# Optimization experiments

Hardware: AMD Instinct MI355X
Metric: run time of the kernel (lower is better)

The kernel has to match this reference:

```python
import jax, jax.numpy as jnp
import numpy as np

N, E, D, H = 50000, 800000, 128, 4

def setup_inputs() -> dict:
    key = jax.random.key(0)
    ks = jax.random.split(key, 6)
    x = jax.random.normal(ks[0], (N, D), dtype=jnp.float32)
    edge_index = jax.random.randint(ks[1], (2, E), 0, N, dtype=jnp.int64)
    W = jax.random.normal(ks[2], (D, H * D), dtype=jnp.float32) * (1.0 / np.sqrt(D))
    att_src = jax.random.normal(ks[3], (H, D), dtype=jnp.float32) * 0.1
    att_dst = jax.random.normal(ks[4], (H, D), dtype=jnp.float32) * 0.1
    bias = jnp.zeros((D,), dtype=jnp.float32)
    gamma = jnp.ones((D,), dtype=jnp.float32)
    beta = jnp.zeros((D,), dtype=jnp.float32)
    return {"x": x, "edge_index": edge_index, "W": W, "att_src": att_src,
            "att_dst": att_dst, "bias": bias, "gamma": gamma, "beta": beta}

def reference(x, edge_index, W, att_src, att_dst, bias, gamma, beta):
    src, dst = edge_index[0], edge_index[1]
    # GATConv: linear transform per head -> [N, H, D]
    xw = (x @ W).reshape(N, H, D)
    a_src = jnp.einsum('nhd,hd->nh', xw, att_src)  # [N, H]
    a_dst = jnp.einsum('nhd,hd->nh', xw, att_dst)  # [N, H]
    alpha = a_src[src] + a_dst[dst]                # [E, H]
    alpha = jax.nn.leaky_relu(alpha, negative_slope=0.2)
    # segment softmax over incoming edges of each dst node
    m = jax.ops.segment_max(alpha, dst, num_segments=N)   # [N, H]
    ex = jnp.exp(alpha - m[dst])                            # [E, H]
    denom = jax.ops.segment_sum(ex, dst, num_segments=N)   # [N, H]
    attn = ex / denom[dst]                                  # [E, H]
    msg = xw[src] * attn[:, :, None]                        # [E, H, D]
    agg = jax.ops.segment_sum(msg, dst, num_segments=N)    # [N, H, D]
    out = agg.mean(axis=1) + bias                           # concat=False: mean heads
    # LayerNorm (eps=1e-5)
    mu = out.mean(axis=-1, keepdims=True)
    var = out.var(axis=-1, keepdims=True)
    out = (out - mu) * jax.lax.rsqrt(var + 1e-5) * gamma + beta
    out = jax.nn.gelu(out, approximate=False)
    return out + x  # project is Identity (in_channels == out_channels)
```

## Files before the change

### kernel.cpp

```cpp
#include <hip/hip_runtime.h>
#include <hip/hip_bf16.h>
#include <hip/hip_fp16.h>
#include <math.h>

#define ND 128
#define NH 4
#define HD 512

typedef __attribute__((ext_vector_type(8))) short bf16x8;
typedef __attribute__((ext_vector_type(4))) float f32x4;

__device__ __forceinline__ unsigned pack_bf16(float a, float b) {
    unsigned ua = __float_as_uint(a), ub = __float_as_uint(b);
    ua = (ua + 0x7fffu + ((ua >> 16) & 1u)) >> 16;
    ub = (ub + 0x7fffu + ((ub >> 16) & 1u)) >> 16;
    return ua | (ub << 16);
}
__device__ __forceinline__ unsigned short bf16r(float a) {
    unsigned ua = __float_as_uint(a);
    return (unsigned short)((ua + 0x7fffu + ((ua >> 16) & 1u)) >> 16);
}
__device__ __forceinline__ float bflo(unsigned u) { return __uint_as_float(u << 16); }
__device__ __forceinline__ float bfhi(unsigned u) { return __uint_as_float(u & 0xffff0000u); }
__device__ __forceinline__ unsigned pack_half2(float a, float b) {
    __half ha = __float2half(a), hb = __float2half(b);
    return (unsigned)__half_as_ushort(ha) | ((unsigned)__half_as_ushort(hb) << 16);
}
__device__ __forceinline__ float2 h22f(unsigned u) {
    __half2 h = *(__half2*)&u;
    return __half22float2(h);
}

__global__ __launch_bounds__(256) void prep_misc(const float* __restrict__ W,
                                                 const float* __restrict__ att_src,
                                                 const float* __restrict__ att_dst,
                                                 unsigned short* __restrict__ Ws,
                                                 float* __restrict__ pt,
                                                 const int* __restrict__ dst,
                                                 int* __restrict__ cnt, int ne) {
    int b = blockIdx.x;
    if (b < 256) {
        int idx = b * 256 + threadIdx.x;
        int j = idx >> 9, K = idx & 511;
        int h = K >> 7, k = K & 127;
        Ws[idx] = bf16r(W[(size_t)k * HD + h * ND + j]);
    } else if (b == 256) {
        int k = threadIdx.x;
        if (k < ND) {
            for (int h = 0; h < NH; ++h) {
                float ps = 0.f, pd = 0.f;
                for (int d = 0; d < ND; ++d) {
                    float wv = W[(size_t)k * HD + h * ND + d];
                    ps = fmaf(wv, att_src[h * ND + d], ps);
                    pd = fmaf(wv, att_dst[h * ND + d], pd);
                }
                pt[h * ND + k] = ps;
                pt[(4 + h) * ND + k] = pd;
            }
        }
    } else {
        int e = (b - 257) * 256 + threadIdx.x;
        if (e < ne) atomicAdd(&cnt[dst[e]], 1);
    }
}

__global__ __launch_bounds__(256) void ka_scanA(const float* __restrict__ x,
                                                const float* __restrict__ pt,
                                                unsigned* __restrict__ xb,
                                                float* __restrict__ a_src,
                                                float* __restrict__ a_dst,
                                                const int* __restrict__ cnt,
                                                int* __restrict__ partial,
                                                int* __restrict__ bsum,
                                                int n, int nbA) {
    __shared__ float pl[8 * ND];
    __shared__ int sh[256];
    if ((int)blockIdx.x < nbA) {
        { int t = threadIdx.x; ((float4*)pl)[t] = ((const float4*)pt)[t]; }
        __syncthreads();
        int wave = (blockIdx.x * 256 + threadIdx.x) >> 6;
        int lane = threadIdx.x & 63;
        if (wave >= n) return;
        float2 xv = ((const float2*)(x + (size_t)wave * ND))[lane];
        xb[(size_t)wave * 64 + lane] = pack_bf16(xv.x, xv.y);
#pragma unroll
        for (int o = 0; o < 8; ++o) {
            float2 pv = ((const float2*)(pl + o * ND))[lane];
            float v = xv.x * pv.x + xv.y * pv.y;
#pragma unroll
            for (int off = 1; off < 64; off <<= 1) v += __shfl_xor(v, off);
            if (lane == 0) {
                if (o < 4) a_src[(size_t)wave * NH + o] = v;
                else       a_dst[(size_t)wave * NH + (o - 4)] = v;
            }
        }
    } else {
        int bid = blockIdx.x - nbA;
        int gid = bid * 256 + threadIdx.x;
        int v = (gid < n) ? cnt[gid] : 0;
        int val = v;
        sh[threadIdx.x] = val;
        __syncthreads();
#pragma unroll
        for (int off = 1; off < 256; off <<= 1) {
            int add = (threadIdx.x >= off) ? sh[threadIdx.x - off] : 0;
            __syncthreads();
            val += add;
            sh[threadIdx.x] = val;
            __syncthreads();
        }
        if (gid < n) partial[gid] = val - v;
        if (threadIdx.x == 255) bsum[bid] = val;
    }
}

__global__ __launch_bounds__(256) void scanBC(const int* __restrict__ partial,
                                              const int* __restrict__ bsum,
                                              int* __restrict__ starts,
                                              int* __restrict__ cursor,
                                              int n, int ne, int nb) {
    __shared__ int sh[256];
    int t = threadIdx.x;
    int v = (t < nb) ? bsum[t] : 0;
    int val = v;
    sh[t] = val;
    __syncthreads();
#pragma unroll
    for (int off = 1; off < 256; off <<= 1) {
        int add = (t >= off) ? sh[t - off] : 0;
        __syncthreads();
        val += add;
        sh[t] = val;
        __syncthreads();
    }
    int myoff = (blockIdx.x == 0) ? 0 : sh[blockIdx.x - 1];
    int gid = blockIdx.x * 256 + t;
    if (gid < n) {
        int s = partial[gid] + myoff;
        starts[gid] = s;
        cursor[gid] = s;
    }
    if (gid == 0) starts[n] = ne;
}

__global__ __launch_bounds__(256) void scatter_edges_w(const int* __restrict__ src,
                                                       const int* __restrict__ dst,
                                                       const float* __restrict__ a_src,
                                                       const float* __restrict__ a_dst,
                                                       int* __restrict__ cursor,
                                                       uint4* __restrict__ eperm, int ne) {
    int e = blockIdx.x * 256 + threadIdx.x;
    if (e < ne) {
        int s = src[e], t = dst[e];
        float4 as = *(const float4*)(a_src + (size_t)s * NH);
        float4 ad = *(const float4*)(a_dst + (size_t)t * NH);
        float A0 = as.x + ad.x, A1 = as.y + ad.y, A2 = as.z + ad.z, A3 = as.w + ad.w;
        A0 = (A0 > 0.f) ? A0 : 0.2f * A0;
        A1 = (A1 > 0.f) ? A1 : 0.2f * A1;
        A2 = (A2 > 0.f) ? A2 : 0.2f * A2;
        A3 = (A3 > 0.f) ? A3 : 0.2f * A3;
        float e0 = expf(A0), e1 = expf(A1), e2 = expf(A2), e3 = expf(A3);
        int pos = atomicAdd(&cursor[t], 1);
        uint4 ev;
        ev.x = (unsigned)s;
        ev.y = pack_half2(e0, e1);
        ev.z = pack_half2(e2, e3);
        ev.w = 0u;
        eperm[pos] = ev;
    }
}

#define FMA16()                                                            \
    { float f0 = bflo(xv.x), f1 = bfhi(xv.x), f2 = bflo(xv.y), f3 = bfhi(xv.y); \
      acc[0] = fmaf(w01.x, f0, acc[0]);  acc[1] = fmaf(w01.x, f1, acc[1]);  \
      acc[2] = fmaf(w01.x, f2, acc[2]);  acc[3] = fmaf(w01.x, f3, acc[3]);  \
      acc[4] = fmaf(w01.y, f0, acc[4]);  acc[5] = fmaf(w01.y, f1, acc[5]);  \
      acc[6] = fmaf(w01.y, f2, acc[6]);  acc[7] = fmaf(w01.y, f3, acc[7]);  \
      acc[8] = fmaf(w23.x, f0, acc[8]);  acc[9] = fmaf(w23.x, f1, acc[9]);  \
      acc[10] = fmaf(w23.x, f2, acc[10]); acc[11] = fmaf(w23.x, f3, acc[11]); \
      acc[12] = fmaf(w23.y, f0, acc[12]); acc[13] = fmaf(w23.y, f1, acc[13]); \
      acc[14] = fmaf(w23.y, f2, acc[14]); acc[15] = fmaf(w23.y, f3, acc[15]); }

__global__ __launch_bounds__(256) void node_agg_fused(
        const uint4* __restrict__ eperm, const int* __restrict__ starts,
        const uint2* __restrict__ xb2, const unsigned short* __restrict__ Ws,
        const float* __restrict__ x, const float* __restrict__ bias,
        const float* __restrict__ gamma, const float* __restrict__ beta,
        float* __restrict__ out, int n) {
    __shared__ char lds[16384];

    const int w = threadIdx.x >> 6;
    const int lane = threadIdx.x & 63;
    const int slot = lane & 31;
    const int half = lane >> 5;
    const int node0 = blockIdx.x * 16;

    for (int i = 0; i < 4; ++i) {
        const int nl = w * 4 + i;
        const int node = node0 + nl;
        int s0 = 0, s1 = 0;
        if (node < n) { s0 = starts[node]; s1 = starts[node + 1]; }

        float den0 = 0.f, den1 = 0.f, den2 = 0.f, den3 = 0.f;
        float acc[16];
#pragma unroll
        for (int j = 0; j < 16; ++j) acc[j] = 0.f;

        for (int base = s0; base < s1; base += 16) {
            int rem = s1 - base; if (rem > 16) rem = 16;
            uint4 ev = {0u, 0u, 0u, 0u};
            if (lane < rem) ev = eperm[base + lane];
            {
                float2 dl = h22f(ev.y), dh = h22f(ev.z);
                den0 += dl.x; den1 += dl.y; den2 += dh.x; den3 += dh.y;
            }
            if (rem == 16) {
#pragma unroll
                for (int pp = 0; pp < 8; ++pp) {
                    int j2 = 2 * pp + half;
                    int s = __shfl((int)ev.x, j2);
                    unsigned uy = __shfl(ev.y, j2);
                    unsigned uz = __shfl(ev.z, j2);
                    uint2 xv = xb2[(size_t)s * 32 + slot];
                    float2 w01 = h22f(uy), w23 = h22f(uz);
                    FMA16();
                }
            } else {
                for (int jj = 0; jj < rem; jj += 2) {
                    int j2 = jj + half;
                    bool valid = (j2 < rem);
                    int j2c = valid ? j2 : jj;
                    int s = __shfl((int)ev.x, j2c);
                    unsigned uy = __shfl(ev.y, j2c);
                    unsigned uz = __shfl(ev.z, j2c);
                    uint2 xv = xb2[(size_t)s * 32 + slot];
                    float2 w01 = h22f(uy), w23 = h22f(uz);
                    float m = valid ? 1.f : 0.f;
                    w01.x *= m; w01.y *= m; w23.x *= m; w23.y *= m;
                    FMA16();
                }
            }
        }

#pragma unroll
        for (int off = 1; off < 64; off <<= 1) {
            den0 += __shfl_xor(den0, off);
            den1 += __shfl_xor(den1, off);
            den2 += __shfl_xor(den2, off);
            den3 += __shfl_xor(den3, off);
        }
        float i0 = (den0 > 0.f) ? 0.25f / den0 : 0.f;
        float i1 = (den1 > 0.f) ? 0.25f / den1 : 0.f;
        float i2 = (den2 > 0.f) ? 0.25f / den2 : 0.f;
        float i3 = (den3 > 0.f) ? 0.25f / den3 : 0.f;

        float v[16];
#pragma unroll
        for (int f = 0; f < 4; ++f) {
            v[0 + f]  = acc[0 + f]  * i0;
            v[4 + f]  = acc[4 + f]  * i1;
            v[8 + f]  = acc[8 + f]  * i2;
            v[12 + f] = acc[12 + f] * i3;
        }
#pragma unroll
        for (int j = 0; j < 16; ++j) v[j] += __shfl_xor(v[j], 32);

#pragma unroll
        for (int hh = 0; hh < 2; ++hh) {
            int h = half * 2 + hh;
            int Kb = (h * ND + slot * 4) * 2;
            int boff = nl * 1024 + ((Kb & ~15) ^ ((nl & 7) << 4)) + (Kb & 8);
            uint2 val;
            val.x = pack_bf16(v[h * 4 + 0], v[h * 4 + 1]);
            val.y = pack_bf16(v[h * 4 + 2], v[h * 4 + 3]);
            *(uint2*)(lds + boff) = val;
        }
    }
    __syncthreads();

    const int g16 = lane >> 4;
    const int e16 = lane & 15;
    f32x4 cacc[2];
    cacc[0] = (f32x4){0.f, 0.f, 0.f, 0.f};
    cacc[1] = (f32x4){0.f, 0.f, 0.f, 0.f};
#pragma unroll
    for (int t = 0; t < 16; ++t) {
        int K0 = t * 32 + 8 * g16;
        bf16x8 a = *(const bf16x8*)(lds + e16 * 1024 + ((K0 * 2) ^ ((e16 & 7) << 4)));
#pragma unroll
        for (int c2 = 0; c2 < 2; ++c2) {
            int c = w * 2 + c2;
            bf16x8 b = *(const bf16x8*)(Ws + (size_t)(c * 16 + e16) * HD + K0);
            cacc[c2] = __builtin_amdgcn_mfma_f32_16x16x32_bf16(a, b, cacc[c2], 0, 0, 0);
        }
    }
    __syncthreads();

    float* C = (float*)lds;
#pragma unroll
    for (int c2 = 0; c2 < 2; ++c2)
#pragma unroll
        for (int ri = 0; ri < 4; ++ri)
            C[(g16 * 4 + ri) * 128 + (w * 2 + c2) * 16 + e16] = cacc[c2][ri];
    __syncthreads();

    float2 bv = ((const float2*)bias)[lane];
    float2 gv = ((const float2*)gamma)[lane];
    float2 tb = ((const float2*)beta)[lane];
    for (int i = 0; i < 4; ++i) {
        int row = w * 4 + i;
        int grow = node0 + row;
        if (grow >= n) break;
        float2 c2v = ((float2*)(C + row * 128))[lane];
        c2v.x += bv.x; c2v.y += bv.y;
        float s = c2v.x + c2v.y, s2 = c2v.x * c2v.x + c2v.y * c2v.y;
#pragma unroll
        for (int off = 1; off < 64; off <<= 1) {
            s += __shfl_xor(s, off);
            s2 += __shfl_xor(s2, off);
        }
        float mu = s * (1.0f / ND);
        float var = s2 * (1.0f / ND) - mu * mu;
        var = fmaxf(var, 0.0f);
        float inv = rsqrtf(var + 1e-5f);
        float2 xres = ((const float2*)(x + (size_t)grow * ND))[lane];
        float y0 = (c2v.x - mu) * inv * gv.x + tb.x;
        float y1 = (c2v.y - mu) * inv * gv.y + tb.y;
        y0 = 0.5f * y0 * (1.0f + erff(y0 * 0.70710678118654752f)) + xres.x;
        y1 = 0.5f * y1 * (1.0f + erff(y1 * 0.70710678118654752f)) + xres.y;
        float2 ov = {y0, y1};
        ((float2*)(out + (size_t)grow * ND))[lane] = ov;
    }
}

extern "C" void kernel_launch(void* const* d_in, const int* in_sizes, int n_in,
                              void* d_out, int out_size, void* d_ws, size_t ws_size,
                              hipStream_t stream) {
    const float* x       = (const float*)d_in[0];
    const int*   edge    = (const int*)d_in[1];
    const float* W       = (const float*)d_in[2];
    const float* att_src = (const float*)d_in[3];
    const float* att_dst = (const float*)d_in[4];
    const float* bias    = (const float*)d_in[5];
    const float* gamma   = (const float*)d_in[6];
    const float* beta    = (const float*)d_in[7];
    float* out = (float*)d_out;

    const int n  = in_sizes[0] / ND;
    const int ne = in_sizes[1] / 2;
    const int* src = edge;
    const int* dst = edge + ne;

    const int nb  = (n + 255) / 256;
    const int nbA = (n + 3) / 4;

    char* wsp = (char*)d_ws;
    unsigned* xb        = (unsigned*)wsp;        wsp += (size_t)n * 64 * sizeof(unsigned);
    unsigned short* Ws  = (unsigned short*)wsp;  wsp += (size_t)ND * HD * sizeof(short);
    float* pt      = (float*)wsp;               wsp += (size_t)8 * ND * sizeof(float);
    float* a_src   = (float*)wsp;               wsp += (size_t)n * NH * sizeof(float);
    float* a_dst   = (float*)wsp;               wsp += (size_t)n * NH * sizeof(float);
    uint4* eperm   = (uint4*)wsp;               wsp += (size_t)ne * sizeof(uint4);
    int*   cnt     = (int*)wsp;                 wsp += (size_t)n * sizeof(int);
    int*   partial = (int*)wsp;                 wsp += (size_t)n * sizeof(int);
    int*   bsum    = (int*)wsp;                 wsp += 256 * sizeof(int);
    int*   starts  = (int*)wsp;                 wsp += (size_t)(n + 1) * sizeof(int);
    int*   cursor  = (int*)wsp;                 wsp += (size_t)n * sizeof(int);

    (void)hipMemsetAsync(cnt, 0, (size_t)n * sizeof(int), stream);

    prep_misc<<<257 + (ne + 255) / 256, 256, 0, stream>>>(W, att_src, att_dst,
                                                          Ws, pt, dst, cnt, ne);

    ka_scanA<<<nbA + nb, 256, 0, stream>>>(x, pt, xb, a_src, a_dst,
                                           cnt, partial, bsum, n, nbA);

    scanBC<<<nb, 256, 0, stream>>>(partial, bsum, starts, cursor, n, ne, nb);

    scatter_edges_w<<<(ne + 255) / 256, 256, 0, stream>>>(src, dst, a_src, a_dst,
                                                          cursor, eperm, ne);

    node_agg_fused<<<(n + 15) / 16, 256, 0, stream>>>(eperm, starts, (const uint2*)xb,
                                                      Ws, x, bias, gamma, beta, out, n);
}
```

Measured before the change: 256.2 us.

## Split fused aggregation+GEMM into separate node aggregation and MFMA GEMM kernels

The fused kernel that aggregated 16 nodes per block into LDS and then ran an MFMA projection is split in two. node_agg now handles one node per wave and writes the bf16 aggregated features to a global buffer. A separate gemm_out kernel then does a 64-row MFMA GEMM with LayerNorm, GELU and the residual in registers. This removes the per-block syncs and LDS staging, and each wave finishes independently instead of waiting on degree imbalance within a block. The cost is an extra n×512 bf16 round trip through global memory (about 51 MB) plus one more launch. The exp in the edge scatter is also switched to the fast __expf.

```diff
diff --git a/kernel.cpp b/kernel.cpp
--- a/kernel.cpp
+++ b/kernel.cpp
@@ -159,7 +159,7 @@
         A1 = (A1 > 0.f) ? A1 : 0.2f * A1;
         A2 = (A2 > 0.f) ? A2 : 0.2f * A2;
         A3 = (A3 > 0.f) ? A3 : 0.2f * A3;
-        float e0 = expf(A0), e1 = expf(A1), e2 = expf(A2), e3 = expf(A3);
+        float e0 = __expf(A0), e1 = __expf(A1), e2 = __expf(A2), e3 = __expf(A3);
         int pos = atomicAdd(&cursor[t], 1);
         uint4 ev;
         ev.x = (unsigned)s;
@@ -181,155 +181,156 @@
       acc[12] = fmaf(w23.y, f0, acc[12]); acc[13] = fmaf(w23.y, f1, acc[13]); \
       acc[14] = fmaf(w23.y, f2, acc[14]); acc[15] = fmaf(w23.y, f3, acc[15]); }
 
-__global__ __launch_bounds__(256) void node_agg_fused(
-        const uint4* __restrict__ eperm, const int* __restrict__ starts,
-        const uint2* __restrict__ xb2, const unsigned short* __restrict__ Ws,
+__global__ __launch_bounds__(256) void node_agg(const uint4* __restrict__ eperm,
+                                                const int* __restrict__ starts,
+                                                const uint2* __restrict__ xb2,
+                                                unsigned* __restrict__ u, int n) {
+    int node = (blockIdx.x * 256 + threadIdx.x) >> 6;
+    int lane = threadIdx.x & 63;
+    if (node >= n) return;
+    const int slot = lane & 31;
+    const int half = lane >> 5;
+
+    int s0 = starts[node], s1 = starts[node + 1];
+
+    float den0 = 0.f, den1 = 0.f, den2 = 0.f, den3 = 0.f;
+    float acc[16];
+#pragma unroll
+    for (int j = 0; j < 16; ++j) acc[j] = 0.f;
+
+    for (int base = s0; base < s1; base += 16) {
+        int rem = s1 - base; if (rem > 16) rem = 16;
+        uint4 ev = {0u, 0u, 0u, 0u};
+        if (lane < rem) ev = eperm[base + lane];
+        {
+            float2 dl = h22f(ev.y), dh = h22f(ev.z);
+            den0 += dl.x; den1 += dl.y; den2 += dh.x; den3 += dh.y;
+        }
+        if (rem == 16) {
+#pragma unroll
+            for (int pp = 0; pp < 8; ++pp) {
+                int j2 = 2 * pp + half;
+                int s = __shfl((int)ev.x, j2);
+                unsigned uy = __shfl(ev.y, j2);
+                unsigned uz = __shfl(ev.z, j2);
+                uint2 xv = xb2[(size_t)s * 32 + slot];
+                float2 w01 = h22f(uy), w23 = h22f(uz);
+                FMA16();
+            }
+        } else {
+            for (int jj = 0; jj < rem; jj += 2) {
+                int j2 = jj + half;
+                bool valid = (j2 < rem);
+                int j2c = valid ? j2 : jj;
+                int s = __shfl((int)ev.x, j2c);
+                unsigned uy = __shfl(ev.y, j2c);
+                unsigned uz = __shfl(ev.z, j2c);
+                uint2 xv = xb2[(size_t)s * 32 + slot];
+                float2 w01 = h22f(uy), w23 = h22f(uz);
+                float m = valid ? 1.f : 0.f;
+                w01.x *= m; w01.y *= m; w23.x *= m; w23.y *= m;
+                FMA16();
+            }
+        }
+    }
+
+#pragma unroll
+    for (int off = 1; off < 64; off <<= 1) {
+        den0 += __shfl_xor(den0, off);
+        den1 += __shfl_xor(den1, off);
+        den2 += __shfl_xor(den2, off);
+        den3 += __shfl_xor(den3, off);
+    }
+    float i0 = (den0 > 0.f) ? 0.25f / den0 : 0.f;
+    float i1 = (den1 > 0.f) ? 0.25f / den1 : 0.f;
+    float i2 = (den2 > 0.f) ? 0.25f / den2 : 0.f;
+    float i3 = (den3 > 0.f) ? 0.25f / den3 : 0.f;
+
+    float v[16];
+#pragma unroll
+    for (int f = 0; f < 4; ++f) {
+        v[0 + f]  = acc[0 + f]  * i0;
+        v[4 + f]  = acc[4 + f]  * i1;
+        v[8 + f]  = acc[8 + f]  * i2;
+        v[12 + f] = acc[12 + f] * i3;
+    }
+#pragma unroll
+    for (int j = 0; j < 16; ++j) v[j] += __shfl_xor(v[j], 32);
+
+#pragma unroll
+    for (int hh = 0; hh < 2; ++hh) {
+        int h = half * 2 + hh;
+        uint2 val;
+        val.x = pack_bf16(v[h * 4 + 0], v[h * 4 + 1]);
+        val.y = pack_bf16(v[h * 4 + 2], v[h * 4 + 3]);
+        ((uint2*)u)[(size_t)node * 128 + h * 32 + slot] = val;
+    }
+}
+
+__global__ __launch_bounds__(256) void gemm_out(
+        const unsigned short* __restrict__ u, const unsigned short* __restrict__ Ws,
         const float* __restrict__ x, const float* __restrict__ bias,
         const float* __restrict__ gamma, const float* __restrict__ beta,
         float* __restrict__ out, int n) {
-    __shared__ char lds[16384];
-
-    const int w = threadIdx.x >> 6;
-    const int lane = threadIdx.x & 63;
-    const int slot = lane & 31;
-    const int half = lane >> 5;
-    const int node0 = blockIdx.x * 16;
-
-    for (int i = 0; i < 4; ++i) {
-        const int nl = w * 4 + i;
-        const int node = node0 + nl;
-        int s0 = 0, s1 = 0;
-        if (node < n) { s0 = starts[node]; s1 = starts[node + 1]; }
-
-        float den0 = 0.f, den1 = 0.f, den2 = 0.f, den3 = 0.f;
-        float acc[16];
-#pragma unroll
-        for (int j = 0; j < 16; ++j) acc[j] = 0.f;
-
-        for (int base = s0; base < s1; base += 16) {
-            int rem = s1 - base; if (rem > 16) rem = 16;
-            uint4 ev = {0u, 0u, 0u, 0u};
-            if (lane < rem) ev = eperm[base + lane];
-            {
-                float2 dl = h22f(ev.y), dh = h22f(ev.z);
-                den0 += dl.x; den1 += dl.y; den2 += dh.x; den3 += dh.y;
-            }
-            if (rem == 16) {
-#pragma unroll
-                for (int pp = 0; pp < 8; ++pp) {
-                    int j2 = 2 * pp + half;
-                    int s = __shfl((int)ev.x, j2);
-                    unsigned uy = __shfl(ev.y, j2);
-                    unsigned uz = __shfl(ev.z, j2);
-                    uint2 xv = xb2[(size_t)s * 32 + slot];
-                    float2 w01 = h22f(uy), w23 = h22f(uz);
-                    FMA16();
-                }
-            } else {
-                for (int jj = 0; jj < rem; jj += 2) {
-                    int j2 = jj + half;
-                    bool valid = (j2 < rem);
-                    int j2c = valid ? j2 : jj;
-                    int s = __shfl((int)ev.x, j2c);
-                    unsigned uy = __shfl(ev.y, j2c);
-                    unsigned uz = __shfl(ev.z, j2c);
-                    uint2 xv = xb2[(size_t)s * 32 + slot];
-                    float2 w01 = h22f(uy), w23 = h22f(uz);
-                    float m = valid ? 1.f : 0.f;
-                    w01.x *= m; w01.y *= m; w23.x *= m; w23.y *= m;
-                    FMA16();
-                }
-            }
-        }
-
-#pragma unroll
-        for (int off = 1; off < 64; off <<= 1) {
-            den0 += __shfl_xor(den0, off);
-            den1 += __shfl_xor(den1, off);
-            den2 += __shfl_xor(den2, off);
-            den3 += __shfl_xor(den3, off);
-        }
-        float i0 = (den0 > 0.f) ? 0.25f / den0 : 0.f;
-        float i1 = (den1 > 0.f) ? 0.25f / den1 : 0.f;
-        float i2 = (den2 > 0.f) ? 0.25f / den2 : 0.f;
-        float i3 = (den3 > 0.f) ? 0.25f / den3 : 0.f;
-
-        float v[16];
-#pragma unroll
-        for (int f = 0; f < 4; ++f) {
-            v[0 + f]  = acc[0 + f]  * i0;
-            v[4 + f]  = acc[4 + f]  * i1;
-            v[8 + f]  = acc[8 + f]  * i2;
-            v[12 + f] = acc[12 + f] * i3;
-        }
-#pragma unroll
-        for (int j = 0; j < 16; ++j) v[j] += __shfl_xor(v[j], 32);
-
-#pragma unroll
-        for (int hh = 0; hh < 2; ++hh) {
-            int h = half * 2 + hh;
-            int Kb = (h * ND + slot * 4) * 2;
-            int boff = nl * 1024 + ((Kb & ~15) ^ ((nl & 7) << 4)) + (Kb & 8);
-            uint2 val;
-            val.x = pack_bf16(v[h * 4 + 0], v[h * 4 + 1]);
-            val.y = pack_bf16(v[h * 4 + 2], v[h * 4 + 3]);
-            *(uint2*)(lds + boff) = val;
-        }
-    }
-    __syncthreads();
-
-    const int g16 = lane >> 4;
-    const int e16 = lane & 15;
-    f32x4 cacc[2];
-    cacc[0] = (f32x4){0.f, 0.f, 0.f, 0.f};
-    cacc[1] = (f32x4){0.f, 0.f, 0.f, 0.f};
-#pragma unroll
-    for (int t = 0; t < 16; ++t) {
-        int K0 = t * 32 + 8 * g16;
-        bf16x8 a = *(const bf16x8*)(lds + e16 * 1024 + ((K0 * 2) ^ ((e16 & 7) << 4)));
-#pragma unroll
-        for (int c2 = 0; c2 < 2; ++c2) {
-            int c = w * 2 + c2;
-            bf16x8 b = *(const bf16x8*)(Ws + (size_t)(c * 16 + e16) * HD + K0);
-            cacc[c2] = __builtin_amdgcn_mfma_f32_16x16x32_bf16(a, b, cacc[c2], 0, 0, 0);
-        }
-    }
-    __syncthreads();
-
-    float* C = (float*)lds;
-#pragma unroll
-    for (int c2 = 0; c2 < 2; ++c2)
-#pragma unroll
-        for (int ri = 0; ri < 4; ++ri)
-            C[(g16 * 4 + ri) * 128 + (w * 2 + c2) * 16 + e16] = cacc[c2][ri];
-    __syncthreads();
-
-    float2 bv = ((const float2*)bias)[lane];
-    float2 gv = ((const float2*)gamma)[lane];
-    float2 tb = ((const float2*)beta)[lane];
-    for (int i = 0; i < 4; ++i) {
-        int row = w * 4 + i;
-        int grow = node0 + row;
-        if (grow >= n) break;
-        float2 c2v = ((float2*)(C + row * 128))[lane];
-        c2v.x += bv.x; c2v.y += bv.y;
-        float s = c2v.x + c2v.y, s2 = c2v.x * c2v.x + c2v.y * c2v.y;
-#pragma unroll
-        for (int off = 1; off < 64; off <<= 1) {
+    const int t = threadIdx.x;
+    const int w = t >> 6, l = t & 63;
+    const int e16 = l & 15, g16 = l >> 4;
+    const int row0 = blockIdx.x * 64 + w * 16;
+
+    int arow = row0 + e16; if (arow >= n) arow = n - 1;
+    const unsigned short* ap = u + (size_t)arow * HD + g16 * 8;
+    const unsigned short* bp[8];
+#pragma unroll
+    for (int c = 0; c < 8; ++c) bp[c] = Ws + (size_t)(c * 16 + e16) * HD + g16 * 8;
+
+    f32x4 acc[8];
+#pragma unroll
+    for (int c = 0; c < 8; ++c) acc[c] = (f32x4){0.f, 0.f, 0.f, 0.f};
+
+#pragma unroll 4
+    for (int ks = 0; ks < 16; ++ks) {
+        bf16x8 a = *(const bf16x8*)(ap + ks * 32);
+#pragma unroll
+        for (int c = 0; c < 8; ++c) {
+            bf16x8 b = *(const bf16x8*)(bp[c] + ks * 32);
+            acc[c] = __builtin_amdgcn_mfma_f32_16x16x32_bf16(a, b, acc[c], 0, 0, 0);
+        }
+    }
+
+    float bias_l[8], gam_l[8], bet_l[8];
+#pragma unroll
+    for (int c = 0; c < 8; ++c) {
+        bias_l[c] = bias[c * 16 + e16];
+        gam_l[c]  = gamma[c * 16 + e16];
+        bet_l[c]  = beta[c * 16 + e16];
+    }
+#pragma unroll
+    for (int ri = 0; ri < 4; ++ri) {
+        int grow = row0 + g16 * 4 + ri;
+        float val[8];
+        float s = 0.f, s2 = 0.f;
+#pragma unroll
+        for (int c = 0; c < 8; ++c) {
+            val[c] = acc[c][ri] + bias_l[c];
+            s += val[c]; s2 += val[c] * val[c];
+        }
+#pragma unroll
+        for (int off = 1; off < 16; off <<= 1) {
             s += __shfl_xor(s, off);
             s2 += __shfl_xor(s2, off);
         }
         float mu = s * (1.0f / ND);
-        float var = s2 * (1.0f / ND) - mu * mu;
-        var = fmaxf(var, 0.0f);
+        float var = fmaxf(s2 * (1.0f / ND) - mu * mu, 0.0f);
         float inv = rsqrtf(var + 1e-5f);
-        float2 xres = ((const float2*)(x + (size_t)grow * ND))[lane];
-        float y0 = (c2v.x - mu) * inv * gv.x + tb.x;
-        float y1 = (c2v.y - mu) * inv * gv.y + tb.y;
-        y0 = 0.5f * y0 * (1.0f + erff(y0 * 0.70710678118654752f)) + xres.x;
-        y1 = 0.5f * y1 * (1.0f + erff(y1 * 0.70710678118654752f)) + xres.y;
-        float2 ov = {y0, y1};
-        ((float2*)(out + (size_t)grow * ND))[lane] = ov;
+        if (grow < n) {
+#pragma unroll
+            for (int c = 0; c < 8; ++c) {
+                float y = (val[c] - mu) * inv * gam_l[c] + bet_l[c];
+                y = 0.5f * y * (1.0f + erff(y * 0.70710678118654752f));
+                out[(size_t)grow * ND + c * 16 + e16] =
+                    y + x[(size_t)grow * ND + c * 16 + e16];
+            }
+        }
     }
 }
 
@@ -356,6 +357,7 @@
 
     char* wsp = (char*)d_ws;
     unsigned* xb        = (unsigned*)wsp;        wsp += (size_t)n * 64 * sizeof(unsigned);
+    unsigned short* u   = (unsigned short*)wsp;  wsp += (size_t)n * HD * sizeof(short);
     unsigned short* Ws  = (unsigned short*)wsp;  wsp += (size_t)ND * HD * sizeof(short);
     float* pt      = (float*)wsp;               wsp += (size_t)8 * ND * sizeof(float);
     float* a_src   = (float*)wsp;               wsp += (size_t)n * NH * sizeof(float);
@@ -380,6 +382,8 @@
     scatter_edges_w<<<(ne + 255) / 256, 256, 0, stream>>>(src, dst, a_src, a_dst,
                                                           cursor, eperm, ne);
 
-    node_agg_fused<<<(n + 15) / 16, 256, 0, stream>>>(eperm, starts, (const uint2*)xb,
-                                                      Ws, x, bias, gamma, beta, out, n);
-}
+    node_agg<<<(n + 3) / 4, 256, 0, stream>>>(eperm, starts, (const uint2*)xb,
+                                              (unsigned*)u, n);
+
+    gemm_out<<<(n + 63) / 64, 256, 0, stream>>>(u, Ws, x, bias, gamma, beta, out, n);
+}
```

Result: slower. 280.5 us (+9.5%).
